# Kernel tuning notes

Hardware: AMD Instinct MI355X
Metric: run time of the kernel (lower is better)

The kernel has to match this reference:

```python
import jax, jax.numpy as jnp
import numpy as np

B, D, K = 32, 64, 26      # batch, n_objects, per-object feature dim
QST = 256                  # question embedding size
G = [512, 512, 512, 512, 512, 512, 28]  # g_layers (last = n_answers)
IN = 2 * K                 # in_size = concat(x_i, x_j)
AGG = 4                    # aggregation + question injection position


def setup_inputs() -> dict:
    key = jax.random.key(0)
    ks = jax.random.split(key, 2 + 2 * len(G))
    inp = {
        "x": jax.random.normal(ks[0], (B, D, K), jnp.float32),
        "qst": jax.random.normal(ks[1], (B, QST), jnp.float32),
    }
    prev = IN
    for i, g in enumerate(G):
        d_in = prev + (QST if i == AGG else 0)
        inp[f"W{i}"] = jax.random.normal(ks[2 + 2 * i], (g, d_in), jnp.float32) * (1.0 / np.sqrt(d_in))
        inp[f"b{i}"] = jnp.zeros((g,), jnp.float32)
        prev = g
    return inp


def reference(x, qst, W0, b0, W1, b1, W2, b2, W3, b3, W4, b4, W5, b5, W6, b6):
    b, d, k = x.shape
    # all ordered pairs: x_full[b, p, q] = [x[b, q], x[b, p]]  (matches torch repeat/cat order)
    xi = jnp.broadcast_to(x[:, None, :, :], (b, d, d, k))
    xj = jnp.broadcast_to(x[:, :, None, :], (b, d, d, k))
    h = jnp.concatenate([xi, xj], axis=-1).reshape(b * d * d, 2 * k)
    Ws = [W0, W1, W2, W3, W4, W5, W6]
    bs = [b0, b1, b2, b3, b4, b5, b6]
    n = len(Ws)
    for i in range(n):
        if i == AGG:
            # sum-aggregation over all d^2 pairs, then question injection
            h = h.reshape(b, d * d, h.shape[-1]).sum(axis=1)  # [b, g]
            h = jnp.concatenate([h, qst], axis=1)             # [b, g+qst]
        h = h @ Ws[i].T + bs[i]
        if i != n - 1:
            h = jax.nn.relu(h)
    return jax.nn.log_softmax(h, axis=1)
```

## Files before the change

kernel.cpp:

```cpp
#include <hip/hip_runtime.h>
#include <math.h>


typedef __attribute__((ext_vector_type(8))) short bf16x8;
typedef __attribute__((ext_vector_type(4))) float f32x4;
typedef __attribute__((ext_vector_type(4))) unsigned int u32x4;

__device__ __forceinline__ unsigned short f2bf(float f) {
    union { float f; unsigned u; } x; x.f = f;
    unsigned r = x.u + 0x7fffu + ((x.u >> 16) & 1u);
    return (unsigned short)(r >> 16);
}

#define NPV_WP   98304
#define NPV_W0P  4096
#define NPV_W4   98304
#define NPV_W5   65536
#define NPV_TOTAL (NPV_WP + NPV_W0P + NPV_W4 + NPV_W5)
__global__ void k_prep(const float* __restrict__ W1, const float* __restrict__ W2,
                       const float* __restrict__ W3, const float* __restrict__ W0,
                       const float* __restrict__ W4, const float* __restrict__ W5,
                       unsigned short* __restrict__ Wp,
                       unsigned short* __restrict__ W0p,
                       float* __restrict__ W4v,
                       float* __restrict__ W5v)
{
    int f = blockIdx.x * 256 + threadIdx.x;
    if (f < NPV_WP) {
        int l = f >> 15, r = f & 32767;
        int n = r >> 6, kq = r & 63;
        const float* W = (l == 0) ? W1 : (l == 1) ? W2 : W3;
        const float* src = W + n * 512 + kq * 8;
        int s = kq >> 2, q4 = kq & 3;
        int wv = n >> 6, jj = (n >> 4) & 3, i16 = n & 15;
        int lane = q4 * 16 + i16;
        unsigned w[4];
        #pragma unroll
        for (int h = 0; h < 4; ++h)
            w[h] = (unsigned)f2bf(src[h * 2]) | ((unsigned)f2bf(src[h * 2 + 1]) << 16);
        *(u32x4*)(Wp + (size_t)l * 262144 + ((((wv * 16 + s) * 4 + jj) * 64 + lane) << 3))
            = (u32x4){w[0], w[1], w[2], w[3]};
    } else if (f < NPV_WP + NPV_W0P) {
        int g = f - NPV_WP;
        int n = g >> 3, kq = g & 7;
        int s = kq >> 2, q4 = kq & 3;
        int wv = n >> 6, jj = (n >> 4) & 3, i16 = n & 15;
        int lane = q4 * 16 + i16;
        unsigned w[4];
        #pragma unroll
        for (int h = 0; h < 4; ++h) {
            int k0 = kq * 8 + h * 2, k1 = k0 + 1;
            float f0 = (k0 < 52) ? W0[n * 52 + k0] : 0.f;
            float f1 = (k1 < 52) ? W0[n * 52 + k1] : 0.f;
            w[h] = (unsigned)f2bf(f0) | ((unsigned)f2bf(f1) << 16);
        }
        *(u32x4*)(W0p + ((((wv * 2 + s) * 4 + jj) * 64 + lane) << 3))
            = (u32x4){w[0], w[1], w[2], w[3]};
    } else if (f < NPV_WP + NPV_W0P + NPV_W4) {
        int g = f - (NPV_WP + NPV_W0P);
        int o = g / 192, kb = g % 192;
        float4 w = *(const float4*)(W4 + (size_t)o * 768 + kb * 4);
        *(float4*)(W4v + (size_t)kb * 2048 + o * 4) = w;
    } else {
        int g = f - (NPV_WP + NPV_W0P + NPV_W4);
        int o = g >> 7, kb = g & 127;
        float4 w = *(const float4*)(W5 + (size_t)o * 512 + kb * 4);
        *(float4*)(W5v + (size_t)kb * 2048 + o * 4) = w;
    }
}

__device__ __forceinline__ void store_h(const f32x4 (&acc)[4][4], const float* __restrict__ bl,
                                        unsigned short* hbuf, int wave, int i16, int q4, int lane)
{
    char* base = (char*)hbuf;
    #pragma unroll
    for (int j = 0; j < 4; ++j) {
        int col = (wave * 4 + j) * 16 + i16;
        int g = col >> 3;
        int e = g & 7;
        float bb = bl[col];
        char* colbase = base + g * 1024 + ((col & 7) << 1);
        #pragma unroll
        for (int mt = 0; mt < 4; ++mt) {
            #pragma unroll
            for (int r = 0; r < 4; ++r) {
                int row = mt * 16 + q4 * 4 + r;
                float v = fmaxf(acc[mt][j][r] + bb, 0.f);
                int vi = __float_as_int(v);
                int swi = __builtin_amdgcn_update_dpp(0, vi, 0xB1, 0xF, 0xF, true);
                if ((lane & 1) == 0) {
                    unsigned pk;
                    asm("v_cvt_pk_bf16_f32 %0, %1, %2" : "=v"(pk) : "v"(vi), "v"(swi));
                    int slot = row ^ e;
                    *(unsigned*)(colbase + slot * 16) = pk;
                }
            }
        }
    }
}

#define CLUSTER(AV0, AV1, AV2, AV3, BV, JJ)                                              \
    __builtin_amdgcn_s_setprio(1);                                                      \
    acc[0][JJ] = __builtin_amdgcn_mfma_f32_16x16x32_bf16(AV0, BV, acc[0][JJ], 0, 0, 0); \
    acc[1][JJ] = __builtin_amdgcn_mfma_f32_16x16x32_bf16(AV1, BV, acc[1][JJ], 0, 0, 0); \
    acc[2][JJ] = __builtin_amdgcn_mfma_f32_16x16x32_bf16(AV2, BV, acc[2][JJ], 0, 0, 0); \
    acc[3][JJ] = __builtin_amdgcn_mfma_f32_16x16x32_bf16(AV3, BV, acc[3][JJ], 0, 0, 0); \
    __builtin_amdgcn_s_setprio(0);                                                      \
    __builtin_amdgcn_sched_barrier(0);

__global__ __launch_bounds__(512, 2) void k_fused(
    const float* __restrict__ x,
    const unsigned short* __restrict__ Wp,
    const unsigned short* __restrict__ W0p,
    const float* __restrict__ b0, const float* __restrict__ b1,
    const float* __restrict__ b2, const float* __restrict__ b3,
    float* __restrict__ P)
{
    __shared__ __align__(16) unsigned short hsm[2 * 64 * 512];
    __shared__ __align__(16) unsigned short xs[8 * 64 * 8];
    int t = threadIdx.x;
    int blk = blockIdx.x;
    int b = blk >> 6, p = blk & 63;

    {
        int row = t >> 3, gr = t & 7;
        const float* xq = x + (size_t)(b * 64 + row) * 26;
        const float* xp = x + (size_t)(b * 64 + p) * 26;
        unsigned w[4];
        #pragma unroll
        for (int h = 0; h < 4; ++h) {
            int k0 = gr * 8 + h * 2;
            int k1 = k0 + 1;
            float f0 = (k0 < 26) ? xq[k0] : (k0 < 52 ? xp[k0 - 26] : 0.f);
            float f1 = (k1 < 26) ? xq[k1] : (k1 < 52 ? xp[k1 - 26] : 0.f);
            w[h] = (unsigned)f2bf(f0) | ((unsigned)f2bf(f1) << 16);
        }
        *(u32x4*)((char*)xs + gr * 1024 + ((row ^ gr) << 4)) = (u32x4){w[0], w[1], w[2], w[3]};
    }

    int wave = t >> 6, lane = t & 63;
    int i16 = lane & 15, q4 = lane >> 4;

    f32x4 acc[4][4];
    bf16x8 X0, X1, X2, X3, Y0, Y1, Y2, Y3;

    const unsigned short* Bb0base = Wp + wave * 32768 + lane * 8;

    __syncthreads();

    {
        #pragma unroll
        for (int mt = 0; mt < 4; ++mt)
            #pragma unroll
            for (int j = 0; j < 4; ++j)
                acc[mt][j] = (f32x4){0.f, 0.f, 0.f, 0.f};
        const unsigned short* Bw0 = W0p + wave * 4096 + lane * 8;
        const char* xb = (const char*)xs;
        #pragma unroll
        for (int s = 0; s < 2; ++s) {
            bf16x8 bfr[4];
            #pragma unroll
            for (int j = 0; j < 4; ++j)
                bfr[j] = *(const bf16x8*)(Bw0 + s * 2048 + j * 512);
            int g = s * 4 + q4;
            const char* A0 = xb + g * 1024 + ((i16 ^ g) << 4);
            #pragma unroll
            for (int mt = 0; mt < 4; ++mt) {
                bf16x8 a = *(const bf16x8*)(A0 + mt * 256);
                #pragma unroll
                for (int j = 0; j < 4; ++j)
                    acc[mt][j] = __builtin_amdgcn_mfma_f32_16x16x32_bf16(a, bfr[j], acc[mt][j], 0, 0, 0);
            }
        }
        X0 = *(const bf16x8*)(Bb0base);
        X1 = *(const bf16x8*)(Bb0base + 512);
        X2 = *(const bf16x8*)(Bb0base + 1024);
        X3 = *(const bf16x8*)(Bb0base + 1536);
        Y0 = *(const bf16x8*)(Bb0base + 2048);
        Y1 = *(const bf16x8*)(Bb0base + 2560);
        Y2 = *(const bf16x8*)(Bb0base + 3072);
        Y3 = *(const bf16x8*)(Bb0base + 3584);
        store_h(acc, b0, hsm, wave, i16, q4, lane);
    }
    __syncthreads();

    int A_even = (q4 << 10) + ((i16 ^ q4) << 4);
    int A_odd  = 4096 + (A_even ^ 64);

    #pragma unroll 1
    for (int l = 0; l < 3; ++l) {
        const float* bl = (l == 0) ? b1 : (l == 1) ? b2 : b3;
        const unsigned short* Bb = Bb0base + (size_t)l * 262144;
        const char* hb = (const char*)hsm + (l & 1) * 65536;
        const char* hbe = hb + A_even;
        const char* hbo = hb + A_odd;

        #pragma unroll
        for (int mt = 0; mt < 4; ++mt)
            #pragma unroll
            for (int j = 0; j < 4; ++j)
                acc[mt][j] = (f32x4){0.f, 0.f, 0.f, 0.f};

        bf16x8 aE0 = *(const bf16x8*)(hbe);
        bf16x8 aE1 = *(const bf16x8*)(hbe + 256);
        bf16x8 aE2 = *(const bf16x8*)(hbe + 512);
        bf16x8 aE3 = *(const bf16x8*)(hbe + 768);
        bf16x8 aO0, aO1, aO2, aO3;

        #pragma unroll 1
        for (int s = 0; s < 16; s += 2) {
            {
                const unsigned short* BX = Bb + ((s + 2 < 16) ? (s + 2) : 14) * 2048;
                const char* po = hbo + (s << 12);
                CLUSTER(aE0, aE1, aE2, aE3, X0, 0)
                X0 = *(const bf16x8*)(BX);
                aO0 = *(const bf16x8*)(po);
                aO1 = *(const bf16x8*)(po + 256);
                CLUSTER(aE0, aE1, aE2, aE3, X1, 1)
                X1 = *(const bf16x8*)(BX + 512);
                aO2 = *(const bf16x8*)(po + 512);
                aO3 = *(const bf16x8*)(po + 768);
                CLUSTER(aE0, aE1, aE2, aE3, X2, 2)
                X2 = *(const bf16x8*)(BX + 1024);
                CLUSTER(aE0, aE1, aE2, aE3, X3, 3)
                X3 = *(const bf16x8*)(BX + 1536);
            }
            {
                const unsigned short* BY = Bb + ((s + 3 < 16) ? (s + 3) : 15) * 2048;
                const char* pe = hbe + ((s + 2 < 16 ? s + 2 : 14) << 12);
                CLUSTER(aO0, aO1, aO2, aO3, Y0, 0)
                Y0 = *(const bf16x8*)(BY);
                aE0 = *(const bf16x8*)(pe);
                aE1 = *(const bf16x8*)(pe + 256);
                CLUSTER(aO0, aO1, aO2, aO3, Y1, 1)
                Y1 = *(const bf16x8*)(BY + 512);
                aE2 = *(const bf16x8*)(pe + 512);
                aE3 = *(const bf16x8*)(pe + 768);
                CLUSTER(aO0, aO1, aO2, aO3, Y2, 2)
                Y2 = *(const bf16x8*)(BY + 1024);
                CLUSTER(aO0, aO1, aO2, aO3, Y3, 3)
                Y3 = *(const bf16x8*)(BY + 1536);
            }
        }

        if (l < 2) {
            const unsigned short* Bn = Bb + 262144;
            X0 = *(const bf16x8*)(Bn);
            X1 = *(const bf16x8*)(Bn + 512);
            X2 = *(const bf16x8*)(Bn + 1024);
            X3 = *(const bf16x8*)(Bn + 1536);
            Y0 = *(const bf16x8*)(Bn + 2048);
            Y1 = *(const bf16x8*)(Bn + 2560);
            Y2 = *(const bf16x8*)(Bn + 3072);
            Y3 = *(const bf16x8*)(Bn + 3584);
            store_h(acc, bl, (unsigned short*)((char*)hsm + ((l + 1) & 1) * 65536),
                    wave, i16, q4, lane);
            __syncthreads();
        } else {
            #pragma unroll
            for (int j = 0; j < 4; ++j) {
                int col = (wave * 4 + j) * 16 + i16;
                float bb = bl[col];
                float sum = 0.f;
                #pragma unroll
                for (int mt = 0; mt < 4; ++mt)
                    #pragma unroll
                    for (int r = 0; r < 4; ++r)
                        sum += fmaxf(acc[mt][j][r] + bb, 0.f);
                sum += __shfl_xor(sum, 16);
                sum += __shfl_xor(sum, 32);
                if (q4 == 0) P[(size_t)blk * 512 + col] = sum;
            }
        }
    }
}

__global__ __launch_bounds__(1024) void k_tail(
    const float* __restrict__ P, const float* __restrict__ qst,
    const float* __restrict__ W4v, const float* __restrict__ b4,
    const float* __restrict__ W5v, const float* __restrict__ b5,
    const float* __restrict__ W6, const float* __restrict__ b6,
    float* __restrict__ out)
{
    int b = blockIdx.x, t = threadIdx.x;
    __shared__ __align__(16) float z[768];
    __shared__ __align__(16) float ps[1024];
    __shared__ __align__(16) float h4[512];
    __shared__ float h5[512];
    __shared__ float logits[28];
    __shared__ float red[2];

    if (t < 512) {
        float s = 0.f;
        const float* Pb = P + (size_t)b * 64 * 512 + t;
        #pragma unroll 8
        for (int c = 0; c < 64; ++c) s += Pb[c * 512];
        z[t] = s;
    } else if (t < 768) {
        z[t] = qst[b * 256 + (t - 512)];
    }
    __syncthreads();
    {
        int o = t & 511, hf = t >> 9;
        float acc = 0.f;
        const float4* Wv = (const float4*)W4v;
        const float4* z4 = (const float4*)z;
        #pragma unroll 4
        for (int kb = hf * 96; kb < hf * 96 + 96; ++kb) {
            float4 w = Wv[kb * 512 + o];
            float4 zz = z4[kb];
            acc = fmaf(w.x, zz.x, acc);
            acc = fmaf(w.y, zz.y, acc);
            acc = fmaf(w.z, zz.z, acc);
            acc = fmaf(w.w, zz.w, acc);
        }
        ps[t] = acc;
    }
    __syncthreads();
    if (t < 512) h4[t] = fmaxf(ps[t] + ps[t + 512] + b4[t], 0.f);
    __syncthreads();
    {
        int o = t & 511, hf = t >> 9;
        float acc = 0.f;
        const float4* Wv = (const float4*)W5v;
        const float4* h44 = (const float4*)h4;
        #pragma unroll 4
        for (int kb = hf * 64; kb < hf * 64 + 64; ++kb) {
            float4 w = Wv[kb * 512 + o];
            float4 hh = h44[kb];
            acc = fmaf(w.x, hh.x, acc);
            acc = fmaf(w.y, hh.y, acc);
            acc = fmaf(w.z, hh.z, acc);
            acc = fmaf(w.w, hh.w, acc);
        }
        ps[t] = acc;
    }
    __syncthreads();
    if (t < 512) h5[t] = fmaxf(ps[t] + ps[t + 512] + b5[t], 0.f);
    __syncthreads();
    {
        int o = t >> 5, c = t & 31;
        if (o < 28) {
            float acc = 0.f;
            for (int k = c; k < 512; k += 32) acc = fmaf(W6[o * 512 + k], h5[k], acc);
            acc += __shfl_xor(acc, 1);
            acc += __shfl_xor(acc, 2);
            acc += __shfl_xor(acc, 4);
            acc += __shfl_xor(acc, 8);
            acc += __shfl_xor(acc, 16);
            if (c == 0) logits[o] = acc + b6[o];
        }
    }
    __syncthreads();
    if (t == 0) {
        float mx = -1e30f;
        for (int cc = 0; cc < 28; ++cc) mx = fmaxf(mx, logits[cc]);
        float se = 0.f;
        for (int cc = 0; cc < 28; ++cc) se += expf(logits[cc] - mx);
        red[0] = mx; red[1] = logf(se);
    }
    __syncthreads();
    if (t < 28) out[b * 28 + t] = logits[t] - red[0] - red[1];
}

extern "C" void kernel_launch(void* const* d_in, const int* in_sizes, int n_in,
                              void* d_out, int out_size, void* d_ws, size_t ws_size,
                              hipStream_t stream)
{
    const float* x   = (const float*)d_in[0];
    const float* qst = (const float*)d_in[1];
    const float* W0  = (const float*)d_in[2];
    const float* b0  = (const float*)d_in[3];
    const float* W1  = (const float*)d_in[4];
    const float* b1  = (const float*)d_in[5];
    const float* W2  = (const float*)d_in[6];
    const float* b2  = (const float*)d_in[7];
    const float* W3  = (const float*)d_in[8];
    const float* b3  = (const float*)d_in[9];
    const float* W4  = (const float*)d_in[10];
    const float* b4  = (const float*)d_in[11];
    const float* W5  = (const float*)d_in[12];
    const float* b5  = (const float*)d_in[13];
    const float* W6  = (const float*)d_in[14];
    const float* b6  = (const float*)d_in[15];
    float* out = (float*)d_out;

    char* ws = (char*)d_ws;
    unsigned short* Wp  = (unsigned short*)(ws);
    unsigned short* W0p = (unsigned short*)(ws + 1572864);
    float*          W4v = (float*)(ws + 1638400);
    float*          W5v = (float*)(ws + 3211264);
    float*          P   = (float*)(ws + 4259840);

    k_prep <<<NPV_TOTAL / 256, 256, 0, stream>>>(W1, W2, W3, W0, W4, W5,
                                                 Wp, W0p, W4v, W5v);
    k_fused<<<2048, 512, 0, stream>>>(x, Wp, W0p, b0, b1, b2, b3, P);
    k_tail <<<32, 1024, 0, stream>>>(P, qst, W4v, b4, W5v, b5, W6, b6, out);
}
```

Baseline: 322.1 us.

## Split tail MLP into four kernels with more blocks per batch

Replaces the single 32-block tail kernel with four kernels: a P reduction, layer 4, layer 5, and the final projection with softmax. Each of the first three runs 256 blocks by splitting output columns eight ways per batch. This spreads the memory-bound weight reads over many more CUs than the previous 32 blocks could use. The cost is three extra kernel launches and round trips of intermediates through global memory.

```diff
diff --git a/kernel.cpp b/kernel.cpp
--- a/kernel.cpp
+++ b/kernel.cpp
@@ -275,79 +275,99 @@
     }
 }
 
-__global__ __launch_bounds__(1024) void k_tail(
-    const float* __restrict__ P, const float* __restrict__ qst,
+__global__ __launch_bounds__(64) void k_t1(const float* __restrict__ P,
+                                           float* __restrict__ Z)
+{
+    int b = blockIdx.x >> 3, sl = blockIdx.x & 7;
+    int col = sl * 64 + threadIdx.x;
+    const float* Pb = P + (size_t)b * 64 * 512 + col;
+    float s = 0.f;
+    #pragma unroll 8
+    for (int c = 0; c < 64; ++c) s += Pb[c * 512];
+    Z[b * 512 + col] = s;
+}
+
+__global__ __launch_bounds__(256) void k_t2(
+    const float* __restrict__ Z, const float* __restrict__ qst,
     const float* __restrict__ W4v, const float* __restrict__ b4,
+    float* __restrict__ H4)
+{
+    int b = blockIdx.x >> 3, sl = blockIdx.x & 7;
+    int t = threadIdx.x;
+    __shared__ __align__(16) float z[768];
+    __shared__ float ps[256];
+    for (int i = t; i < 768; i += 256)
+        z[i] = (i < 512) ? Z[b * 512 + i] : qst[b * 256 + (i - 512)];
+    __syncthreads();
+    int o = sl * 64 + (t & 63), hf = t >> 6;
+    float acc = 0.f;
+    const float4* Wv = (const float4*)W4v;
+    const float4* z4 = (const float4*)z;
+    #pragma unroll 4
+    for (int kb = hf * 48; kb < hf * 48 + 48; ++kb) {
+        float4 w = Wv[kb * 512 + o];
+        float4 zz = z4[kb];
+        acc = fmaf(w.x, zz.x, acc);
+        acc = fmaf(w.y, zz.y, acc);
+        acc = fmaf(w.z, zz.z, acc);
+        acc = fmaf(w.w, zz.w, acc);
+    }
+    ps[t] = acc;
+    __syncthreads();
+    if (t < 64)
+        H4[b * 512 + o] = fmaxf(ps[t] + ps[t + 64] + ps[t + 128] + ps[t + 192] + b4[o], 0.f);
+}
+
+__global__ __launch_bounds__(256) void k_t3(
+    const float* __restrict__ H4,
     const float* __restrict__ W5v, const float* __restrict__ b5,
+    float* __restrict__ H5)
+{
+    int b = blockIdx.x >> 3, sl = blockIdx.x & 7;
+    int t = threadIdx.x;
+    __shared__ __align__(16) float h4[512];
+    __shared__ float ps[256];
+    for (int i = t; i < 512; i += 256) h4[i] = H4[b * 512 + i];
+    __syncthreads();
+    int o = sl * 64 + (t & 63), hf = t >> 6;
+    float acc = 0.f;
+    const float4* Wv = (const float4*)W5v;
+    const float4* h44 = (const float4*)h4;
+    #pragma unroll 4
+    for (int kb = hf * 32; kb < hf * 32 + 32; ++kb) {
+        float4 w = Wv[kb * 512 + o];
+        float4 hh = h44[kb];
+        acc = fmaf(w.x, hh.x, acc);
+        acc = fmaf(w.y, hh.y, acc);
+        acc = fmaf(w.z, hh.z, acc);
+        acc = fmaf(w.w, hh.w, acc);
+    }
+    ps[t] = acc;
+    __syncthreads();
+    if (t < 64)
+        H5[b * 512 + o] = fmaxf(ps[t] + ps[t + 64] + ps[t + 128] + ps[t + 192] + b5[o], 0.f);
+}
+
+__global__ __launch_bounds__(512) void k_t4(
+    const float* __restrict__ H5,
     const float* __restrict__ W6, const float* __restrict__ b6,
     float* __restrict__ out)
 {
     int b = blockIdx.x, t = threadIdx.x;
-    __shared__ __align__(16) float z[768];
-    __shared__ __align__(16) float ps[1024];
-    __shared__ __align__(16) float h4[512];
-    __shared__ float h5[512];
+    __shared__ __align__(16) float h5[512];
     __shared__ float logits[28];
     __shared__ float red[2];
-
-    if (t < 512) {
-        float s = 0.f;
-        const float* Pb = P + (size_t)b * 64 * 512 + t;
-        #pragma unroll 8
-        for (int c = 0; c < 64; ++c) s += Pb[c * 512];
-        z[t] = s;
-    } else if (t < 768) {
-        z[t] = qst[b * 256 + (t - 512)];
-    }
+    h5[t] = H5[b * 512 + t];
     __syncthreads();
     {
-        int o = t & 511, hf = t >> 9;
-        float acc = 0.f;
-        const float4* Wv = (const float4*)W4v;
-        const float4* z4 = (const float4*)z;
-        #pragma unroll 4
-        for (int kb = hf * 96; kb < hf * 96 + 96; ++kb) {
-            float4 w = Wv[kb * 512 + o];
-            float4 zz = z4[kb];
-            acc = fmaf(w.x, zz.x, acc);
-            acc = fmaf(w.y, zz.y, acc);
-            acc = fmaf(w.z, zz.z, acc);
-            acc = fmaf(w.w, zz.w, acc);
-        }
-        ps[t] = acc;
-    }
-    __syncthreads();
-    if (t < 512) h4[t] = fmaxf(ps[t] + ps[t + 512] + b4[t], 0.f);
-    __syncthreads();
-    {
-        int o = t & 511, hf = t >> 9;
-        float acc = 0.f;
-        const float4* Wv = (const float4*)W5v;
-        const float4* h44 = (const float4*)h4;
-        #pragma unroll 4
-        for (int kb = hf * 64; kb < hf * 64 + 64; ++kb) {
-            float4 w = Wv[kb * 512 + o];
-            float4 hh = h44[kb];
-            acc = fmaf(w.x, hh.x, acc);
-            acc = fmaf(w.y, hh.y, acc);
-            acc = fmaf(w.z, hh.z, acc);
-            acc = fmaf(w.w, hh.w, acc);
-        }
-        ps[t] = acc;
-    }
-    __syncthreads();
-    if (t < 512) h5[t] = fmaxf(ps[t] + ps[t + 512] + b5[t], 0.f);
-    __syncthreads();
-    {
-        int o = t >> 5, c = t & 31;
+        int o = t >> 4, c = t & 15;
         if (o < 28) {
             float acc = 0.f;
-            for (int k = c; k < 512; k += 32) acc = fmaf(W6[o * 512 + k], h5[k], acc);
+            for (int k = c; k < 512; k += 16) acc = fmaf(W6[o * 512 + k], h5[k], acc);
             acc += __shfl_xor(acc, 1);
             acc += __shfl_xor(acc, 2);
             acc += __shfl_xor(acc, 4);
             acc += __shfl_xor(acc, 8);
-            acc += __shfl_xor(acc, 16);
             if (c == 0) logits[o] = acc + b6[o];
         }
     }
@@ -391,9 +411,15 @@
     float*          W4v = (float*)(ws + 1638400);
     float*          W5v = (float*)(ws + 3211264);
     float*          P   = (float*)(ws + 4259840);
+    float*          Z   = (float*)(ws + 8454144);
+    float*          H4  = (float*)(ws + 8519680);
+    float*          H5  = (float*)(ws + 8585216);
 
     k_prep <<<NPV_TOTAL / 256, 256, 0, stream>>>(W1, W2, W3, W0, W4, W5,
                                                  Wp, W0p, W4v, W5v);
     k_fused<<<2048, 512, 0, stream>>>(x, Wp, W0p, b0, b1, b2, b3, P);
-    k_tail <<<32, 1024, 0, stream>>>(P, qst, W4v, b4, W5v, b5, W6, b6, out);
-}
+    k_t1   <<<256, 64, 0, stream>>>(P, Z);
+    k_t2   <<<256, 256, 0, stream>>>(Z, qst, W4v, b4, H4);
+    k_t3   <<<256, 256, 0, stream>>>(H4, W5v, b5, H5);
+    k_t4   <<<32, 512, 0, stream>>>(H5, W6, b6, out);
+}
```

Measured after the change: 314.2 us (median of 2 runs). -2.4%, faster.
